# Kernel optimization log

Measured on AMD Instinct MI355X. Metric: run time of the kernel, lower is better.

The kernel has to match this reference:

```python
import jax, jax.numpy as jnp
import numpy as np

EPS = 1e-5
P = 2  # polynomial kernel degree


def setup_inputs() -> dict:
    key = jax.random.key(0)
    k1, k2, k3 = jax.random.split(key, 3)
    b, t, h, d = 2, 2048, 8, 64
    Q = jax.random.normal(k1, (b, t, h, d), jnp.float32)
    K = jax.random.normal(k2, (b, t, h, d), jnp.float32)
    V = jax.random.normal(k3, (b, t, h, d), jnp.float32)
    return {"Q": Q, "K": K, "V": V, "chunk_count": 16}


def reference(Q, K, V, chunk_count):
    b, t, h, d = Q.shape
    dv = V.shape[-1]
    c = chunk_count
    n = t // c  # tokens per chunk

    def to_chunked(X):
        # [b, t, h, d] -> [c, b, h, n, d]
        return X.reshape(b, c, n, h, X.shape[-1]).transpose(1, 0, 3, 2, 4)

    Qc, Kc, Vc = to_chunked(Q), to_chunked(K), to_chunked(V)

    # ---- per-chunk states: s = K^T K, S = sum_n (K_n outer K_n) outer V_n ----
    s_loc = jnp.einsum('cbhni,cbhnj->cbhij', Kc, Kc)                 # [c,b,h,d,d]
    S_loc = jnp.einsum('cbhni,cbhnj,cbhnv->cbhijv', Kc, Kc, Vc)      # [c,b,h,d,d,dv]
    # inclusive cumulative merge over chunks
    S = jnp.cumsum(S_loc, axis=0)
    s = jnp.cumsum(s_loc, axis=0)

    # ---- local within-chunk masked quadratic attention ----
    D = jnp.einsum('cbhqi,cbhki->cbhqk', Qc, Kc)                     # [c,b,h,n,n]
    C = D ** P
    mask = jnp.tril(jnp.ones((n, n), dtype=bool))
    B = jnp.where(mask, C, 0.0)
    Y = jnp.einsum('cbhqk,cbhkv->cbhqv', B, Vc)                      # [c,b,h,n,dv]
    Z = B.sum(-1) + EPS                                              # [c,b,h,n]

    # ---- cross-chunk contribution: chunk i>0 attends to state of chunks <i ----
    Qp = Qc[1:]
    Sp, sp = S[:-1], s[:-1]
    num = jnp.einsum('cbhni,cbhnj,cbhijv->cbhnv', Qp, Qp, Sp)
    den = jnp.einsum('cbhni,cbhnj,cbhij->cbhn', Qp, Qp, sp)
    Y = Y.at[1:].add(num)
    Z = Z.at[1:].add(den)

    out = (Y / Z[..., None]).transpose(1, 0, 3, 2, 4).reshape(b, t, h, dv)
    return out
```

## Files before the change

### kernel.cpp

```cpp
#include <hip/hip_runtime.h>
#include <hip/hip_fp16.h>

typedef __attribute__((ext_vector_type(8))) _Float16 f16x8;
typedef __attribute__((ext_vector_type(8))) unsigned short u16x8;
typedef __attribute__((ext_vector_type(4))) float f32x4;

constexpr int NT = 256;
constexpr int TILE_SHORTS = 4096;
constexpr int SSTR = 72;

__device__ __forceinline__ int swzoff(int row, int c) {
    return row * 64 + (((c) ^ (row & 7)) << 3);
}

__device__ __forceinline__ unsigned short f2h_u(float x) {
    return __half_as_ushort(__float2half(x));
}

__global__ __launch_bounds__(256, 4) void prepass(
    const float* __restrict__ Kg, const float* __restrict__ Vg,
    unsigned short* __restrict__ Kw, unsigned short* __restrict__ Vw)
{
    __shared__ __align__(16) float Vl[64 * 68];
    const int tile = blockIdx.x;
    const int bh   = blockIdx.y;
    const int b = bh >> 3, h = bh & 7;
    const int tid = threadIdx.x;
    const size_t gbase = (((size_t)b * 2048 + tile * 64) * 8 + h) * 64;

    #pragma unroll
    for (int j = 0; j < 4; ++j) {
        int id = j * 256 + tid, row = id >> 4, c4 = id & 15;
        *(float4*)&Vl[row * 68 + c4 * 4] =
            *(const float4*)&Vg[gbase + (size_t)row * 512 + c4 * 4];
    }

    unsigned short* Ko = Kw + (size_t)(bh * 32 + tile) * TILE_SHORTS;
    #pragma unroll
    for (int j = 0; j < 2; ++j) {
        int id = j * 256 + tid, row = id >> 3, c = id & 7;
        const float* src = &Kg[gbase + (size_t)row * 512 + c * 8];
        float4 x = *(const float4*)src, y = *(const float4*)(src + 4);
        u16x8 o;
        o[0] = f2h_u(x.x); o[1] = f2h_u(x.y); o[2] = f2h_u(x.z); o[3] = f2h_u(x.w);
        o[4] = f2h_u(y.x); o[5] = f2h_u(y.y); o[6] = f2h_u(y.z); o[7] = f2h_u(y.w);
        *(u16x8*)&Ko[swzoff(row, c)] = o;
    }
    __syncthreads();

    unsigned short* Vo = Vw + (size_t)(bh * 32 + tile) * TILE_SHORTS;
    #pragma unroll
    for (int j = 0; j < 2; ++j) {
        int id = j * 256 + tid, vrow = id >> 3, c = id & 7;
        u16x8 o;
        #pragma unroll
        for (int i = 0; i < 8; ++i) o[i] = f2h_u(Vl[(c * 8 + i) * 68 + vrow]);
        *(u16x8*)&Vo[swzoff(vrow, c)] = o;
    }
}

__global__ __launch_bounds__(NT, 3) void attn_pow2_f16(
    const float* __restrict__ Qg,
    const unsigned short* __restrict__ Kw, const unsigned short* __restrict__ Vw,
    float* __restrict__ Og)
{
    __shared__ __align__(16) unsigned short lds[4 * TILE_SHORTS + 4 * 16 * SSTR];
    unsigned short* const Kb = lds;
    unsigned short* const Vb = lds + 2 * TILE_SHORTS;
    const int tid  = threadIdx.x;
    const int lane = tid & 63;
    const int wave = tid >> 6;
    const int a    = lane & 15;
    const int quad = lane >> 4;
    const int m0   = wave * 16;
    unsigned short* const Sme = lds + 4 * TILE_SHORTS + wave * (16 * SSTR);

    int r0 = (int)blockIdx.x;
    int wr = (r0 < 256) ? r0 : (767 - r0);
    const int qt = 31 - (wr >> 4);
    const int bh = wr & 15;
    const int b = bh >> 3, h = bh & 7;
    const int q0 = qt * 64;

    f16x8 aQ[2];
    {
        const size_t qrowbase = (((size_t)b * 2048 + q0 + m0 + a) * 8 + h) * 64;
        #pragma unroll
        for (int ks = 0; ks < 2; ++ks) {
            const float* src = &Qg[qrowbase + ks * 32 + quad * 8];
            float4 x = *(const float4*)src, y = *(const float4*)(src + 4);
            u16x8 o;
            o[0] = f2h_u(x.x); o[1] = f2h_u(x.y); o[2] = f2h_u(x.z); o[3] = f2h_u(x.w);
            o[4] = f2h_u(y.x); o[5] = f2h_u(y.y); o[6] = f2h_u(y.z); o[7] = f2h_u(y.w);
            aQ[ks] = __builtin_bit_cast(f16x8, o);
        }
    }

    const unsigned short* Ktiles = Kw + (size_t)bh * 32 * TILE_SHORTS;
    const unsigned short* Vtiles = Vw + (size_t)bh * 32 * TILE_SHORTS;

    u16x8 rK[2], rV[2];
    auto gload = [&](int kt) {
        const u16x8* kg = (const u16x8*)(Ktiles + (size_t)kt * TILE_SHORTS);
        const u16x8* vg = (const u16x8*)(Vtiles + (size_t)kt * TILE_SHORTS);
        rK[0] = kg[tid * 2]; rK[1] = kg[tid * 2 + 1];
        rV[0] = vg[tid * 2]; rV[1] = vg[tid * 2 + 1];
    };
    gload(0);

    f32x4 oacc[4];
    #pragma unroll
    for (int n = 0; n < 4; ++n) oacc[n] = (f32x4){0.f, 0.f, 0.f, 0.f};
    float den[4] = {0.f, 0.f, 0.f, 0.f};

    for (int kt = 0; kt <= qt; ++kt) {
        const int buf = kt & 1;
        __syncthreads();

        u16x8* kd = (u16x8*)(Kb + buf * TILE_SHORTS);
        u16x8* vd = (u16x8*)(Vb + buf * TILE_SHORTS);
        kd[tid * 2] = rK[0]; kd[tid * 2 + 1] = rK[1];
        vd[tid * 2] = rV[0]; vd[tid * 2 + 1] = rV[1];
        if (kt < qt) gload(kt + 1);

        __syncthreads();

        const unsigned short* Kc = Kb + buf * TILE_SHORTS;
        const unsigned short* Vc = Vb + buf * TILE_SHORTS;

        f32x4 sacc[4];
        #pragma unroll
        for (int n = 0; n < 4; ++n) sacc[n] = (f32x4){0.f, 0.f, 0.f, 0.f};
        #pragma unroll
        for (int n = 0; n < 4; ++n) {
            #pragma unroll
            for (int ks = 0; ks < 2; ++ks) {
                f16x8 bK = *(const f16x8*)&Kc[swzoff(n * 16 + a, ks * 4 + quad)];
                sacc[n] = __builtin_amdgcn_mfma_f32_16x16x32_f16(aQ[ks], bK, sacc[n], 0, 0, 0);
            }
        }

        const bool diag = (kt == qt);
        #pragma unroll
        for (int n = 0; n < 4; ++n) {
            const int col = n * 16 + a;
            #pragma unroll
            for (int r = 0; r < 4; ++r) {
                float d0 = sacc[n][r];
                float p = d0 * d0;
                if (diag && col > (m0 + quad * 4 + r)) p = 0.f;
                den[r] += p;
                Sme[(quad * 4 + r) * SSTR + col] = f2h_u(p);
            }
        }

        f16x8 aS[2];
        #pragma unroll
        for (int ks = 0; ks < 2; ++ks)
            aS[ks] = *(const f16x8*)&Sme[a * SSTR + ks * 32 + quad * 8];
        #pragma unroll
        for (int n = 0; n < 4; ++n) {
            #pragma unroll
            for (int ks = 0; ks < 2; ++ks) {
                f16x8 bV = *(const f16x8*)&Vc[swzoff(n * 16 + a, ks * 4 + quad)];
                oacc[n] = __builtin_amdgcn_mfma_f32_16x16x32_f16(aS[ks], bV, oacc[n], 0, 0, 0);
            }
        }
    }

    #pragma unroll
    for (int r = 0; r < 4; ++r) {
        den[r] += __shfl_xor(den[r], 1);
        den[r] += __shfl_xor(den[r], 2);
        den[r] += __shfl_xor(den[r], 4);
        den[r] += __shfl_xor(den[r], 8);
    }
    float invz[4];
    #pragma unroll
    for (int r = 0; r < 4; ++r) invz[r] = 1.0f / (den[r] + 1e-5f);

    #pragma unroll
    for (int n = 0; n < 4; ++n) {
        #pragma unroll
        for (int r = 0; r < 4; ++r) {
            int t = q0 + m0 + quad * 4 + r;
            int v = n * 16 + a;
            Og[(((size_t)b * 2048 + t) * 8 + h) * 64 + v] = oacc[n][r] * invz[r];
        }
    }
}

extern "C" void kernel_launch(void* const* d_in, const int* in_sizes, int n_in,
                              void* d_out, int out_size, void* d_ws, size_t ws_size,
                              hipStream_t stream) {
    const float* Q = (const float*)d_in[0];
    const float* K = (const float*)d_in[1];
    const float* V = (const float*)d_in[2];
    float* O = (float*)d_out;
    unsigned short* Kw = (unsigned short*)d_ws;
    unsigned short* Vw = Kw + (size_t)16 * 32 * TILE_SHORTS;

    prepass<<<dim3(32, 16), 256, 0, stream>>>(K, V, Kw, Vw);
    attn_pow2_f16<<<dim3(512), NT, 0, stream>>>(Q, Kw, Vw, O);
}
```

Before: 98.58 us.

## Compute transposed scores so P feeds PV MFMA from registers without LDS

Swaps the QK^T MFMA operands so each lane holds scores in the layout needed as the A operand of 16x16x16 MFMAs. The squared scores are then converted and used straight from registers, which removes the per-wave LDS staging buffer and its write and read round trip. The V prepass permutes its columns to match the new k ordering, and the denominator reduction is reworked for the transposed layout. The loop also drops one barrier per iteration by syncing only after the LDS store. That relies on the double buffer to keep the write to one buffer from racing reads of the previous one, and it uses twice as many smaller MFMAs for PV.

```diff
diff --git a/kernel.cpp b/kernel.cpp
--- a/kernel.cpp
+++ b/kernel.cpp
@@ -2,17 +2,16 @@
 #include <hip/hip_fp16.h>
 
 typedef __attribute__((ext_vector_type(8))) _Float16 f16x8;
+typedef __attribute__((ext_vector_type(4))) _Float16 f16x4;
 typedef __attribute__((ext_vector_type(8))) unsigned short u16x8;
 typedef __attribute__((ext_vector_type(4))) float f32x4;
 
 constexpr int NT = 256;
 constexpr int TILE_SHORTS = 4096;
-constexpr int SSTR = 72;
 
 __device__ __forceinline__ int swzoff(int row, int c) {
-    return row * 64 + (((c) ^ (row & 7)) << 3);
-}
-
+    return row * 64 + ((c ^ (row & 7)) << 3);
+}
 __device__ __forceinline__ unsigned short f2h_u(float x) {
     return __half_as_ushort(__float2half(x));
 }
@@ -51,11 +50,14 @@
     unsigned short* Vo = Vw + (size_t)(bh * 32 + tile) * TILE_SHORTS;
     #pragma unroll
     for (int j = 0; j < 2; ++j) {
-        int id = j * 256 + tid, vrow = id >> 3, c = id & 7;
+        int id = j * 256 + tid, vrow = id >> 3, g = id & 7;
         u16x8 o;
         #pragma unroll
-        for (int i = 0; i < 8; ++i) o[i] = f2h_u(Vl[(c * 8 + i) * 68 + vrow]);
-        *(u16x8*)&Vo[swzoff(vrow, c)] = o;
+        for (int jj = 0; jj < 8; ++jj) {
+            int kk = ((g & 1) * 2 + (jj >> 2)) * 16 + (g >> 1) * 4 + (jj & 3);
+            o[jj] = f2h_u(Vl[kk * 68 + vrow]);
+        }
+        *(u16x8*)&Vo[swzoff(vrow, g)] = o;
     }
 }
 
@@ -64,7 +66,7 @@
     const unsigned short* __restrict__ Kw, const unsigned short* __restrict__ Vw,
     float* __restrict__ Og)
 {
-    __shared__ __align__(16) unsigned short lds[4 * TILE_SHORTS + 4 * 16 * SSTR];
+    __shared__ __align__(16) unsigned short lds[4 * TILE_SHORTS];
     unsigned short* const Kb = lds;
     unsigned short* const Vb = lds + 2 * TILE_SHORTS;
     const int tid  = threadIdx.x;
@@ -73,7 +75,6 @@
     const int a    = lane & 15;
     const int quad = lane >> 4;
     const int m0   = wave * 16;
-    unsigned short* const Sme = lds + 4 * TILE_SHORTS + wave * (16 * SSTR);
 
     int r0 = (int)blockIdx.x;
     int wr = (r0 < 256) ? r0 : (767 - r0);
@@ -82,7 +83,7 @@
     const int b = bh >> 3, h = bh & 7;
     const int q0 = qt * 64;
 
-    f16x8 aQ[2];
+    f16x8 bQ[2];
     {
         const size_t qrowbase = (((size_t)b * 2048 + q0 + m0 + a) * 8 + h) * 64;
         #pragma unroll
@@ -92,7 +93,7 @@
             u16x8 o;
             o[0] = f2h_u(x.x); o[1] = f2h_u(x.y); o[2] = f2h_u(x.z); o[3] = f2h_u(x.w);
             o[4] = f2h_u(y.x); o[5] = f2h_u(y.y); o[6] = f2h_u(y.z); o[7] = f2h_u(y.w);
-            aQ[ks] = __builtin_bit_cast(f16x8, o);
+            bQ[ks] = __builtin_bit_cast(f16x8, o);
         }
     }
 
@@ -111,73 +112,72 @@
     f32x4 oacc[4];
     #pragma unroll
     for (int n = 0; n < 4; ++n) oacc[n] = (f32x4){0.f, 0.f, 0.f, 0.f};
-    float den[4] = {0.f, 0.f, 0.f, 0.f};
+    float den_l = 0.f;
+
+    union U8 { u16x8 u; f16x4 q[2]; };
 
     for (int kt = 0; kt <= qt; ++kt) {
         const int buf = kt & 1;
-        __syncthreads();
-
         u16x8* kd = (u16x8*)(Kb + buf * TILE_SHORTS);
         u16x8* vd = (u16x8*)(Vb + buf * TILE_SHORTS);
         kd[tid * 2] = rK[0]; kd[tid * 2 + 1] = rK[1];
         vd[tid * 2] = rV[0]; vd[tid * 2 + 1] = rV[1];
+        __syncthreads();
         if (kt < qt) gload(kt + 1);
-
-        __syncthreads();
 
         const unsigned short* Kc = Kb + buf * TILE_SHORTS;
         const unsigned short* Vc = Vb + buf * TILE_SHORTS;
 
         f32x4 sacc[4];
         #pragma unroll
-        for (int n = 0; n < 4; ++n) sacc[n] = (f32x4){0.f, 0.f, 0.f, 0.f};
-        #pragma unroll
-        for (int n = 0; n < 4; ++n) {
+        for (int s = 0; s < 4; ++s) sacc[s] = (f32x4){0.f, 0.f, 0.f, 0.f};
+        #pragma unroll
+        for (int s = 0; s < 4; ++s) {
             #pragma unroll
             for (int ks = 0; ks < 2; ++ks) {
-                f16x8 bK = *(const f16x8*)&Kc[swzoff(n * 16 + a, ks * 4 + quad)];
-                sacc[n] = __builtin_amdgcn_mfma_f32_16x16x32_f16(aQ[ks], bK, sacc[n], 0, 0, 0);
+                f16x8 aK = *(const f16x8*)&Kc[swzoff(s * 16 + a, ks * 4 + quad)];
+                sacc[s] = __builtin_amdgcn_mfma_f32_16x16x32_f16(aK, bQ[ks], sacc[s], 0, 0, 0);
             }
         }
 
         const bool diag = (kt == qt);
-        #pragma unroll
-        for (int n = 0; n < 4; ++n) {
-            const int col = n * 16 + a;
+        f16x4 aS[4];
+        #pragma unroll
+        for (int s = 0; s < 4; ++s) {
+            float p[4];
             #pragma unroll
             for (int r = 0; r < 4; ++r) {
-                float d0 = sacc[n][r];
-                float p = d0 * d0;
-                if (diag && col > (m0 + quad * 4 + r)) p = 0.f;
-                den[r] += p;
-                Sme[(quad * 4 + r) * SSTR + col] = f2h_u(p);
+                float d0 = sacc[s][r];
+                float v = d0 * d0;
+                if (diag && (s * 16 + quad * 4 + r) > (m0 + a)) v = 0.f;
+                p[r] = v;
             }
-        }
-
-        f16x8 aS[2];
-        #pragma unroll
-        for (int ks = 0; ks < 2; ++ks)
-            aS[ks] = *(const f16x8*)&Sme[a * SSTR + ks * 32 + quad * 8];
+            den_l += (p[0] + p[1]) + (p[2] + p[3]);
+            aS[s] = (f16x4){(_Float16)p[0], (_Float16)p[1], (_Float16)p[2], (_Float16)p[3]};
+        }
+
         #pragma unroll
         for (int n = 0; n < 4; ++n) {
-            #pragma unroll
-            for (int ks = 0; ks < 2; ++ks) {
-                f16x8 bV = *(const f16x8*)&Vc[swzoff(n * 16 + a, ks * 4 + quad)];
-                oacc[n] = __builtin_amdgcn_mfma_f32_16x16x32_f16(aS[ks], bV, oacc[n], 0, 0, 0);
-            }
-        }
-    }
-
+            const int vrow = n * 16 + a;
+            U8 va, vb;
+            va.u = *(const u16x8*)&Vc[swzoff(vrow, quad * 2)];
+            vb.u = *(const u16x8*)&Vc[swzoff(vrow, quad * 2 + 1)];
+            oacc[n] = __builtin_amdgcn_mfma_f32_16x16x16f16(aS[0], va.q[0], oacc[n], 0, 0, 0);
+            oacc[n] = __builtin_amdgcn_mfma_f32_16x16x16f16(aS[1], va.q[1], oacc[n], 0, 0, 0);
+            oacc[n] = __builtin_amdgcn_mfma_f32_16x16x16f16(aS[2], vb.q[0], oacc[n], 0, 0, 0);
+            oacc[n] = __builtin_amdgcn_mfma_f32_16x16x16f16(aS[3], vb.q[1], oacc[n], 0, 0, 0);
+        }
+    }
+
+    den_l += __shfl_xor(den_l, 16);
+    den_l += __shfl_xor(den_l, 32);
+
+    float invz[4];
     #pragma unroll
     for (int r = 0; r < 4; ++r) {
-        den[r] += __shfl_xor(den[r], 1);
-        den[r] += __shfl_xor(den[r], 2);
-        den[r] += __shfl_xor(den[r], 4);
-        den[r] += __shfl_xor(den[r], 8);
-    }
-    float invz[4];
-    #pragma unroll
-    for (int r = 0; r < 4; ++r) invz[r] = 1.0f / (den[r] + 1e-5f);
+        float dq = __shfl(den_l, quad * 4 + r);
+        invz[r] = 1.0f / (dq + 1e-5f);
+    }
 
     #pragma unroll
     for (int n = 0; n < 4; ++n) {
```

Result: no change. 96.82 us (-1.8%).
